# Kernel tuning notes

Measured on AMD Instinct MI355X. Metric: run time of the kernel, lower is better.

Reference implementation:

```python
import jax, jax.numpy as jnp
import numpy as np

S = 2048          # sequence length (single prefill sequence)
HID = 4096        # hidden_size
NH, NKV, HD = 32, 8, 128   # q heads, kv heads, head_dim
THETA = 10000.0
SCALE = HD ** -0.5


def setup_inputs() -> dict:
    key = jax.random.key(0)
    k1, k2, k3 = jax.random.split(key, 3)
    hidden_states = jax.random.normal(k1, (S, HID), jnp.float32)
    positions = jnp.arange(S, dtype=jnp.int32)
    W_qkv = jax.random.normal(k2, (HID, (NH + 2 * NKV) * HD), jnp.float32) * 0.02
    W_o = jax.random.normal(k3, (NH * HD, HID), jnp.float32) * 0.02
    return {"hidden_states": hidden_states, "positions": positions,
            "W_qkv": W_qkv, "W_o": W_o}


def _rope(x, positions):
    # x: [T, H, HD]; neox-style RoPE (rotate halves, is_neox_style=True)
    half = HD // 2
    inv_freq = 1.0 / (THETA ** (jnp.arange(half, dtype=jnp.float32) / half))
    freqs = positions.astype(jnp.float32)[:, None] * inv_freq[None, :]  # [T, half]
    cos = jnp.cos(freqs)[:, None, :]
    sin = jnp.sin(freqs)[:, None, :]
    x1, x2 = x[..., :half], x[..., half:]
    return jnp.concatenate([x1 * cos - x2 * sin, x2 * cos + x1 * sin], axis=-1)


def reference(hidden_states, positions, W_qkv, W_o):
    # fused QKV projection then split (q_size = NH*HD, kv_size = NKV*HD)
    qkv = hidden_states @ W_qkv                      # [S, (NH+2*NKV)*HD]
    q, k, v = jnp.split(qkv, [NH * HD, NH * HD + NKV * HD], axis=1)
    q = _rope(q.reshape(S, NH, HD), positions)       # [S, NH, HD]
    k = _rope(k.reshape(S, NKV, HD), positions)      # [S, NKV, HD]
    v = v.reshape(S, NKV, HD)
    # GQA: broadcast kv heads to query heads
    rep = NH // NKV
    k = jnp.repeat(k, rep, axis=1)                   # [S, NH, HD]
    v = jnp.repeat(v, rep, axis=1)
    scores = jnp.einsum('qhd,khd->hqk', q, k) * SCALE  # [NH, S, S]
    causal = jnp.tril(jnp.ones((S, S), dtype=bool))
    scores = jnp.where(causal[None], scores, jnp.finfo(scores.dtype).min)
    attn = jax.nn.softmax(scores, axis=-1)
    out = jnp.einsum('hqk,khd->qhd', attn, v).reshape(S, NH * HD)
    return out @ W_o                                 # [S, HID]
```

## Files before the change

kernel.cpp:

```cpp
#include <hip/hip_runtime.h>
#include <math.h>
#include <stdint.h>

#define S_LEN 2048
#define HID 4096
#define NH 32
#define NKV 8
#define HD 128
#define QKV_N ((NH + 2*NKV) * HD)
#define NQK (NH + NKV)
static __device__ __constant__ const float SCALE_F = 0.08838834764831845f;

typedef __bf16 bf16x8 __attribute__((ext_vector_type(8)));
typedef __bf16 bf16x4 __attribute__((ext_vector_type(4)));
typedef float  f32x4  __attribute__((ext_vector_type(4)));
typedef uint32_t u32x4 __attribute__((ext_vector_type(4)));

#define GLD_LDS(gptr, lptr) \
  __builtin_amdgcn_global_load_lds( \
      (const __attribute__((address_space(1))) uint32_t*)(gptr), \
      (__attribute__((address_space(3))) uint32_t*)(lptr), 16, 0, 0)

__device__ __forceinline__ void tp64(const float* __restrict__ in, __bf16* __restrict__ out,
                                     int R, int C, int bx, int by, int tid, float* tile) {
  int lr = tid >> 4;
  int lc = (tid & 15) * 4;
  #pragma unroll
  for (int p = 0; p < 4; ++p) {
    int r = p * 16 + lr;
    const float4 v = *(const float4*)&in[(size_t)(by + r) * C + bx + lc];
    float* t = &tile[r * 65 + lc];
    t[0] = v.x; t[1] = v.y; t[2] = v.z; t[3] = v.w;
  }
  __syncthreads();
  int oc = tid >> 5;
  int orr = (tid & 31) * 2;
  #pragma unroll
  for (int p = 0; p < 8; ++p) {
    int c = p * 8 + oc;
    float v0 = tile[orr * 65 + c];
    float v1 = tile[(orr + 1) * 65 + c];
    __bf16 b2[2] = { (__bf16)v0, (__bf16)v1 };
    *(uint32_t*)&out[(size_t)(bx + c) * R + by + orr] = *(uint32_t*)b2;
  }
}

__global__ __launch_bounds__(256) void fused_prep_kernel(const float* __restrict__ hidden,
                                                         __bf16* __restrict__ hid_bf,
                                                         const float* __restrict__ Wqkv,
                                                         __bf16* __restrict__ wqkvT,
                                                         const float* __restrict__ Wo,
                                                         __bf16* __restrict__ woT) {
  __shared__ float tile[64 * 65];
  const int b = blockIdx.x;
  const int tid = threadIdx.x;
  if (b < 2048) {
    const float4* in4 = (const float4*)hidden;
    int i = b * 256 + tid;
    #pragma unroll
    for (int k = 0; k < 4; ++k) {
      float4 v = in4[i + k * 524288];
      bf16x4 o = { (__bf16)v.x, (__bf16)v.y, (__bf16)v.z, (__bf16)v.w };
      *(bf16x4*)(hid_bf + (size_t)(i + k * 524288) * 4) = o;
    }
  } else if (b < 8192) {
    int id = b - 2048;
    int bx = (id % 96) * 64, by = (id / 96) * 64;
    tp64(Wqkv, wqkvT, HID, QKV_N, bx, by, tid, tile);
  } else {
    int id = b - 8192;
    int bx = (id & 63) * 64, by = (id >> 6) * 64;
    tp64(Wo, woT, HID, HID, bx, by, tid, tile);
  }
}

__global__ __launch_bounds__(256) void fused_rope_tpv_kernel(const __bf16* __restrict__ qkv,
                                                             const int* __restrict__ pos,
                                                             __bf16* __restrict__ Qr,
                                                             __bf16* __restrict__ Kr,
                                                             __bf16* __restrict__ Vt) {
  __shared__ __bf16 tile[32][33];
  const int b = blockIdx.x;
  const int tid = threadIdx.x;
  if (b < 20480) {
    int idx = b * 256 + tid;
    int half = idx & 63;
    int t = idx >> 6;
    int hh = t % NQK;
    int s = t / NQK;
    if (s >= S_LEN) return;
    float p = (float)pos[s];
    float inv_freq = exp2f((float)half * -0.2076205059304601f);
    float ang = p * inv_freq;
    float cs = cosf(ang), sn = sinf(ang);
    const __bf16* src; __bf16* dst;
    if (hh < NH) {
      src = qkv + (size_t)s * QKV_N + (size_t)hh * HD;
      dst = Qr + ((size_t)s * NH + hh) * HD;
    } else {
      int kh = hh - NH;
      src = qkv + (size_t)s * QKV_N + (size_t)NH * HD + (size_t)kh * HD;
      dst = Kr + ((size_t)s * NKV + kh) * HD;
    }
    float x1 = (float)src[half], x2 = (float)src[half + 64];
    dst[half]      = (__bf16)(x1 * cs - x2 * sn);
    dst[half + 64] = (__bf16)(x2 * cs + x1 * sn);
  } else {
    int id = b - 20480;
    int sb = (id & 63) * 32;
    int db = ((id >> 6) & 3) * 32;
    int kvh = id >> 8;
    int tx = tid & 31, ty = tid >> 5;
    const __bf16* src = qkv + (size_t)(NH + NKV) * HD + (size_t)kvh * HD;
    for (int i = 0; i < 32; i += 8)
      tile[ty + i][tx] = src[(size_t)(sb + ty + i) * QKV_N + db + tx];
    __syncthreads();
    for (int i = 0; i < 32; i += 8)
      Vt[((size_t)kvh * HD + db + ty + i) * S_LEN + sb + tx] = tile[tx][ty + i];
  }
}

template <typename OutT>
__global__ __launch_bounds__(512, 2) void gemm8p_kernel(const __bf16* __restrict__ A,
                                                        const __bf16* __restrict__ Bt,
                                                        OutT* __restrict__ C0,
                                                        OutT* __restrict__ C1,
                                                        int M, int N, int Kext, int ld) {
  __shared__ __align__(16) __bf16 sA[2][2][256 * 32];
  __shared__ __align__(16) __bf16 sB[2][2][256 * 32];
  const int tid = threadIdx.x;
  const int lane = tid & 63;
  const int wave = tid >> 6;
  const int quad = lane >> 4;
  const int l16 = lane & 15;
  const int wm = (wave >> 2) * 128;
  const int wn = (wave & 3) * 64;

  const int z = blockIdx.z;
  A += (size_t)z * Kext;
  Bt += (size_t)z * Kext;
  OutT* __restrict__ C = z ? C1 : C0;

  const int nx = gridDim.x;
  size_t bm, bn;
  if (gridDim.y == 8 && (nx & 7) == 0) {
    int lin = blockIdx.y * nx + blockIdx.x;
    int j = lin >> 3, xcd = lin & 7;
    bm = (size_t)(j & 7) * 256;
    bn = (size_t)(xcd * (nx >> 3) + (j >> 3)) * 256;
  } else {
    bm = (size_t)blockIdx.y * 256;
    bn = (size_t)blockIdx.x * 256;
  }

  const int NT = Kext >> 6;
  const int rsw = (l16 >> 1) & 3;

  f32x4 acc[8][4] = {};
  bf16x8 aR[2][4], bR[2][4];

  const int row0 = tid >> 2;
  const int chL = (tid & 3) ^ ((tid >> 3) & 3);
  const uint64_t off128 = (uint64_t)128 * ld * 2;
  uint64_t aGA = (uint64_t)(uintptr_t)A + ((bm + row0) * (size_t)ld) * 2 + (size_t)chL * 16;
  uint64_t bGA = (uint64_t)(uintptr_t)Bt + ((bn + row0) * (size_t)ld) * 2 + (size_t)chL * 16;

  typedef __attribute__((address_space(3))) __bf16 lds_bf16;
  const uint32_t sAb = (uint32_t)(uintptr_t)(lds_bf16*)&sA[0][0][0];
  const uint32_t sBb = (uint32_t)(uintptr_t)(lds_bf16*)&sB[0][0][0];
  const uint32_t wlds = (uint32_t)__builtin_amdgcn_readfirstlane(wave * 1024);
  const uint32_t aBase = sAb + (uint32_t)(((wm + l16) * 32 + (quad ^ rsw) * 8) * 2);
  const uint32_t bBase = sBb + (uint32_t)(((wn + l16) * 32 + (quad ^ rsw) * 8) * 2);

#define LDSA(bf, kk) (sAb + (bf) * 32768u + (kk) * 16384u)
#define LDSB(bf, kk) (sBb + (bf) * 32768u + (kk) * 16384u)

#define STAGE_ASM(ga, ldsbase) \
  asm volatile("s_mov_b32 m0, %0\n\t" \
               "global_load_lds_dwordx4 %2, off\n\t" \
               "s_mov_b32 m0, %1\n\t" \
               "global_load_lds_dwordx4 %3, off" \
               :: "s"((ldsbase) + wlds), "s"((ldsbase) + wlds + 8192u), \
                  "v"(ga), "v"((ga) + off128) : "memory")

#define DSRD4(dst, baseaddr) do {                                                 \
    u32x4 t0_, t1_, t2_, t3_;                                                     \
    asm volatile("ds_read_b128 %0, %4\n\t"                                        \
                 "ds_read_b128 %1, %4 offset:1024\n\t"                            \
                 "ds_read_b128 %2, %4 offset:2048\n\t"                            \
                 "ds_read_b128 %3, %4 offset:3072"                                \
                 : "=&v"(t0_), "=&v"(t1_), "=&v"(t2_), "=&v"(t3_)                 \
                 : "v"(baseaddr));                                                \
    dst[0] = __builtin_bit_cast(bf16x8, t0_);                                     \
    dst[1] = __builtin_bit_cast(bf16x8, t1_);                                     \
    dst[2] = __builtin_bit_cast(bf16x8, t2_);                                     \
    dst[3] = __builtin_bit_cast(bf16x8, t3_);                                     \
  } while (0)

#define ISSUE_A(set, bf, kk, ih) DSRD4(aR[set], aBase + (bf) * 32768u + (kk) * 16384u + (ih) * 4096u)
#define ISSUE_B(set, bf, kk)     DSRD4(bR[set], bBase + (bf) * 32768u + (kk) * 16384u)

#define MFMA16(as, bs, ih) do {                                                   \
    __builtin_amdgcn_s_setprio(1);                                                \
    _Pragma("unroll")                                                             \
    for (int i_ = 0; i_ < 4; ++i_)                                                \
      _Pragma("unroll")                                                           \
      for (int j_ = 0; j_ < 4; ++j_)                                              \
        acc[(ih) * 4 + i_][j_] = __builtin_amdgcn_mfma_f32_16x16x32_bf16(         \
            aR[as][i_], bR[bs][j_], acc[(ih) * 4 + i_][j_], 0, 0, 0);             \
    __builtin_amdgcn_s_setprio(0);                                                \
    __builtin_amdgcn_sched_barrier(0);                                            \
  } while (0)

#define BAR() __builtin_amdgcn_s_barrier()
#define LGKM4() do { asm volatile("s_waitcnt lgkmcnt(4)");                        \
                     __builtin_amdgcn_sched_barrier(0); } while (0)
#define LGKM8() do { asm volatile("s_waitcnt lgkmcnt(8)");                        \
                     __builtin_amdgcn_sched_barrier(0); } while (0)
#define VMCNT4() do { asm volatile("s_waitcnt vmcnt(4)");                         \
                      __builtin_amdgcn_sched_barrier(0); } while (0)

  STAGE_ASM(aGA,        LDSA(0, 0));
  STAGE_ASM(bGA,        LDSB(0, 0));
  STAGE_ASM(aGA + 64,   LDSA(0, 1));
  STAGE_ASM(bGA + 64,   LDSB(0, 1));
  STAGE_ASM(aGA + 128,  LDSA(1, 0));
  STAGE_ASM(bGA + 128,  LDSB(1, 0));
  aGA += 192; bGA += 192;
  asm volatile("s_waitcnt vmcnt(8)");
  __builtin_amdgcn_sched_barrier(0);
  BAR();
  ISSUE_A(0, 0, 0, 0); ISSUE_B(0, 0, 0);

  for (int u = 0; u < (NT >> 1); ++u) {
    VMCNT4();
    ISSUE_A(1, 0, 0, 1);
    BAR();
    LGKM4();
    MFMA16(0, 0, 0);
    STAGE_ASM(aGA, LDSA(1, 1)); aGA += 64;
    ISSUE_A(0, 0, 1, 0); ISSUE_B(1, 0, 1);
    BAR();
    LGKM8();
    MFMA16(1, 0, 1);
    STAGE_ASM(bGA, LDSB(1, 1)); bGA += 64;
    VMCNT4();
    ISSUE_A(1, 0, 1, 1);
    BAR();
    LGKM4();
    MFMA16(0, 1, 0);
    STAGE_ASM(aGA, LDSA(0, 0)); aGA += 64;
    ISSUE_A(0, 1, 0, 0); ISSUE_B(0, 1, 0);
    BAR();
    LGKM8();
    MFMA16(1, 1, 1);
    STAGE_ASM(bGA, LDSB(0, 0)); bGA += 64;
    VMCNT4();
    ISSUE_A(1, 1, 0, 1);
    BAR();
    LGKM4();
    MFMA16(0, 0, 0);
    STAGE_ASM(aGA, LDSA(0, 1)); aGA += 64;
    ISSUE_A(0, 1, 1, 0); ISSUE_B(1, 1, 1);
    BAR();
    LGKM8();
    MFMA16(1, 0, 1);
    STAGE_ASM(bGA, LDSB(0, 1)); bGA += 64;
    VMCNT4();
    ISSUE_A(1, 1, 1, 1);
    BAR();
    LGKM4();
    MFMA16(0, 1, 0);
    STAGE_ASM(aGA, LDSA(1, 0)); aGA += 64;
    ISSUE_A(0, 0, 0, 0); ISSUE_B(0, 0, 0);
    BAR();
    LGKM8();
    MFMA16(1, 1, 1);
    STAGE_ASM(bGA, LDSB(1, 0)); bGA += 64;
  }

  asm volatile("s_waitcnt vmcnt(0) lgkmcnt(0)");
  __builtin_amdgcn_sched_barrier(0);

  #pragma unroll
  for (int i = 0; i < 8; ++i)
    #pragma unroll
    for (int j = 0; j < 4; ++j)
      #pragma unroll
      for (int r = 0; r < 4; ++r) {
        size_t row = bm + wm + i * 16 + quad * 4 + r;
        size_t col = bn + wn + j * 16 + l16;
        C[row * (size_t)N + col] = (OutT)acc[i][j][r];
      }

#undef LDSA
#undef LDSB
#undef STAGE_ASM
#undef DSRD4
#undef ISSUE_A
#undef ISSUE_B
#undef MFMA16
#undef BAR
#undef LGKM4
#undef LGKM8
#undef VMCNT4
}

template <typename OutT>
__global__ __launch_bounds__(512, 2) void gemm128_kernel(const __bf16* __restrict__ A,
                                                         const __bf16* __restrict__ Bt,
                                                         OutT* __restrict__ C,
                                                         int M, int N, int K) {
  __shared__ __align__(16) __bf16 sA[3][2][128 * 32];
  __shared__ __align__(16) __bf16 sB[3][2][256 * 32];
  const int tid = threadIdx.x;
  const int lane = tid & 63;
  const int wave = tid >> 6;
  const int quad = lane >> 4;
  const int l16 = lane & 15;
  const int wm = (wave >> 2) * 64;
  const int wn = (wave & 3) * 64;

  const int nx = gridDim.x, ny = gridDim.y;
  const int nwg = nx * ny;
  int lin = blockIdx.y * nx + blockIdx.x;
  size_t bm, bn;
  if ((nwg & 7) == 0) {
    int swz = (lin & 7) * (nwg >> 3) + (lin >> 3);
    bm = (size_t)(swz % ny) * 128;
    bn = (size_t)(swz / ny) * 256;
  } else {
    bm = (size_t)blockIdx.y * 128;
    bn = (size_t)blockIdx.x * 256;
  }

  const int NT = K >> 6;
  const int rsw = (l16 >> 1) & 3;

  f32x4 acc[4][4] = {};
  bf16x8 aR[2][4], bR[2][4];

  const int rowA = tid >> 2;
  const int chLs = (tid & 3) ^ ((tid >> 3) & 3);
  const uint64_t off128B = (uint64_t)128 * K * 2;
  uint64_t aGA = (uint64_t)(uintptr_t)A + ((bm + rowA) * (size_t)K) * 2 + (size_t)chLs * 16;
  uint64_t bGA = (uint64_t)(uintptr_t)Bt + ((bn + rowA) * (size_t)K) * 2 + (size_t)chLs * 16;

  typedef __attribute__((address_space(3))) __bf16 lds_bf16;
  const uint32_t sAb = (uint32_t)(uintptr_t)(lds_bf16*)&sA[0][0][0];
  const uint32_t sBb = (uint32_t)(uintptr_t)(lds_bf16*)&sB[0][0][0];
  const uint32_t wlds = (uint32_t)__builtin_amdgcn_readfirstlane(wave * 1024);
  const uint32_t aBase = sAb + (uint32_t)(((wm + l16) * 32 + (quad ^ rsw) * 8) * 2);
  const uint32_t bBase = sBb + (uint32_t)(((wn + l16) * 32 + (quad ^ rsw) * 8) * 2);

#define STA128(ga, ldsoff) \
  asm volatile("s_mov_b32 m0, %0\n\t" \
               "global_load_lds_dwordx4 %1, off" \
               :: "s"((ldsoff) + wlds), "v"(ga) : "memory")

#define STB128(ga, ldsoff) \
  asm volatile("s_mov_b32 m0, %0\n\t" \
               "global_load_lds_dwordx4 %2, off\n\t" \
               "s_mov_b32 m0, %1\n\t" \
               "global_load_lds_dwordx4 %3, off" \
               :: "s"((ldsoff) + wlds), "s"((ldsoff) + wlds + 8192u), \
                  "v"(ga), "v"((ga) + off128B) : "memory")

#define DSRD4(dst, baseaddr) do {                                                 \
    u32x4 t0_, t1_, t2_, t3_;                                                     \
    asm volatile("ds_read_b128 %0, %4\n\t"                                        \
                 "ds_read_b128 %1, %4 offset:1024\n\t"                            \
                 "ds_read_b128 %2, %4 offset:2048\n\t"                            \
                 "ds_read_b128 %3, %4 offset:3072"                                \
                 : "=&v"(t0_), "=&v"(t1_), "=&v"(t2_), "=&v"(t3_)                 \
                 : "v"(baseaddr));                                                \
    dst[0] = __builtin_bit_cast(bf16x8, t0_);                                     \
    dst[1] = __builtin_bit_cast(bf16x8, t1_);                                     \
    dst[2] = __builtin_bit_cast(bf16x8, t2_);                                     \
    dst[3] = __builtin_bit_cast(bf16x8, t3_);                                     \
  } while (0)

#define IS_A(set, aoff, kh) DSRD4(aR[set], aBase + (aoff) + (kh) * 8192u)
#define IS_B(set, boff, kh) DSRD4(bR[set], bBase + (boff) + (kh) * 16384u)

#define MFMA16Q(ss) do {                                                          \
    __builtin_amdgcn_s_setprio(1);                                                \
    _Pragma("unroll")                                                             \
    for (int i_ = 0; i_ < 4; ++i_)                                                \
      _Pragma("unroll")                                                           \
      for (int j_ = 0; j_ < 4; ++j_)                                              \
        acc[i_][j_] = __builtin_amdgcn_mfma_f32_16x16x32_bf16(                    \
            aR[ss][i_], bR[ss][j_], acc[i_][j_], 0, 0, 0);                        \
    __builtin_amdgcn_s_setprio(0);                                                \
    __builtin_amdgcn_sched_barrier(0);                                            \
  } while (0)

#define BARX() __builtin_amdgcn_s_barrier()
#define LGKM8X() do { asm volatile("s_waitcnt lgkmcnt(8)");                       \
                      __builtin_amdgcn_sched_barrier(0); } while (0)
#define VMCNT6X() do { asm volatile("s_waitcnt vmcnt(6)");                        \
                       __builtin_amdgcn_sched_barrier(0); } while (0)

  uint32_t curA = 0u, nxtA = 16384u, stgA = 32768u;
  uint32_t curB = 0u, nxtB = 32768u, stgB = 65536u;

  STA128(aGA,       sAb + 0u);
  STA128(aGA + 64,  sAb + 8192u);
  STB128(bGA,       sBb + 0u);
  STB128(bGA + 64,  sBb + 16384u);
  STA128(aGA + 128, sAb + 16384u);
  STA128(aGA + 192, sAb + 16384u + 8192u);
  STB128(bGA + 128, sBb + 32768u);
  STB128(bGA + 192, sBb + 32768u + 16384u);
  aGA += 256; bGA += 256;
  VMCNT6X();
  BARX();
  IS_A(0, curA, 0); IS_B(0, curB, 0);

  for (int t = 0; t < NT; ++t) {
    IS_A(1, curA, 1); IS_B(1, curB, 1);
    STA128(aGA, sAb + stgA);
    STB128(bGA, sBb + stgB);
    LGKM8X();
    MFMA16Q(0);
    STA128(aGA + 64, sAb + stgA + 8192u);
    STB128(bGA + 64, sBb + stgB + 16384u);
    aGA += 128; bGA += 128;
    VMCNT6X();
    BARX();
    IS_A(0, nxtA, 0); IS_B(0, nxtB, 0);
    LGKM8X();
    MFMA16Q(1);
    BARX();
    uint32_t ta = curA; curA = nxtA; nxtA = stgA; stgA = ta;
    uint32_t tb = curB; curB = nxtB; nxtB = stgB; stgB = tb;
  }

  asm volatile("s_waitcnt vmcnt(0) lgkmcnt(0)");
  __builtin_amdgcn_sched_barrier(0);

  #pragma unroll
  for (int i = 0; i < 4; ++i)
    #pragma unroll
    for (int j = 0; j < 4; ++j)
      #pragma unroll
      for (int r = 0; r < 4; ++r) {
        size_t row = bm + wm + i * 16 + quad * 4 + r;
        size_t col = bn + wn + j * 16 + l16;
        C[row * (size_t)N + col] = (OutT)acc[i][j][r];
      }

#undef STA128
#undef STB128
#undef DSRD4
#undef IS_A
#undef IS_B
#undef MFMA16Q
#undef BARX
#undef LGKM8X
#undef VMCNT6X
}

__global__ __launch_bounds__(256, 2) void attn_kernel(const __bf16* __restrict__ Qr,
                                                      const __bf16* __restrict__ Kr,
                                                      const __bf16* __restrict__ Vt,
                                                      __bf16* __restrict__ O) {
  __shared__ __align__(16) char smem[73728];
  __bf16* Ps = (__bf16*)(smem + 65536);

  const int bid = blockIdx.x;
  const int h = bid & (NH - 1);
  const int j = bid >> 5;
  const int qb = (j < 8) ? (15 - j) : (j - 8);
  const int kvh = h >> 2;
  const int tid = threadIdx.x;
  const int lane = tid & 63, wave = tid >> 6;
  const int quad = lane >> 4, l16 = lane & 15;
  const int sw = l16 & 7;
  const int q0 = qb * 128;

#define STAGE_KV(kbase, bufv) do {                                                 \
    char* kd_ = smem + (bufv) * 16384;                                             \
    char* vd_ = smem + 32768 + (bufv) * 16384;                                     \
    _Pragma("unroll")                                                              \
    for (int pass_ = 0; pass_ < 4; ++pass_) {                                      \
      int c_ = pass_ * 256 + tid;                                                  \
      int row_ = c_ >> 4, ch_ = c_ & 15;                                           \
      int chs_ = ch_ ^ (row_ & 7);                                                 \
      GLD_LDS(&Kr[(size_t)((kbase) + row_) * (NKV * HD) + (size_t)kvh * HD + chs_ * 8], \
              kd_ + c_ * 16);                                                      \
    }                                                                              \
    _Pragma("unroll")                                                              \
    for (int pass_ = 0; pass_ < 4; ++pass_) {                                      \
      int c_ = pass_ * 256 + tid;                                                  \
      int d_ = c_ >> 3, ch_ = c_ & 7;                                              \
      int chs_ = ch_ ^ (d_ & 7);                                                   \
      GLD_LDS(&Vt[((size_t)kvh * HD + d_) * S_LEN + (kbase) + chs_ * 8],           \
              vd_ + c_ * 16);                                                      \
    }                                                                              \
  } while (0)

#define SOFTMAX_SET(scX, m2X, liX, oaccX, maskCond, pfX) do {                      \
    float s_[16];                                                                  \
    _Pragma("unroll")                                                              \
    for (int jt_ = 0; jt_ < 4; ++jt_)                                              \
      _Pragma("unroll")                                                            \
      for (int r_ = 0; r_ < 4; ++r_) s_[jt_ * 4 + r_] = scX[jt_][r_];              \
    if (maskCond) {                                                                \
      int qloc_ = wave * 16 + l16;                                                 \
      _Pragma("unroll")                                                            \
      for (int jt_ = 0; jt_ < 4; ++jt_)                                            \
        _Pragma("unroll")                                                          \
        for (int r_ = 0; r_ < 4; ++r_)                                             \
          if (jt_ * 16 + quad * 4 + r_ > qloc_) s_[jt_ * 4 + r_] = -INFINITY;      \
    }                                                                              \
    float mx_ = s_[0];                                                             \
    _Pragma("unroll")                                                              \
    for (int i_ = 1; i_ < 16; ++i_) mx_ = fmaxf(mx_, s_[i_]);                      \
    mx_ = fmaxf(mx_, __shfl_xor(mx_, 16, 64));                                     \
    mx_ = fmaxf(mx_, __shfl_xor(mx_, 32, 64));                                     \
    float mxs_ = mx_ * C2;                                                         \
    if (!__all(mxs_ <= m2X + 11.54f)) {                                            \
      float m2n_ = fmaxf(m2X, mxs_);                                               \
      float al_ = exp2f(m2X - m2n_);                                               \
      liX *= al_;                                                                  \
      _Pragma("unroll")                                                            \
      for (int dt_ = 0; dt_ < 8; ++dt_) oaccX[dt_] *= al_;                         \
      m2X = m2n_;                                                                  \
    }                                                                              \
    float sum_ = 0.0f;                                                             \
    __bf16* pw_ = Ps + wave * 1024 + l16 * 64;                                     \
    _Pragma("unroll")                                                              \
    for (int jt_ = 0; jt_ < 4; ++jt_) {                                            \
      float e0_ = exp2f(fmaf(s_[jt_*4+0], C2, -m2X));                              \
      float e1_ = exp2f(fmaf(s_[jt_*4+1], C2, -m2X));                              \
      float e2_ = exp2f(fmaf(s_[jt_*4+2], C2, -m2X));                              \
      float e3_ = exp2f(fmaf(s_[jt_*4+3], C2, -m2X));                              \
      sum_ += (e0_ + e1_) + (e2_ + e3_);                                           \
      bf16x4 pk_ = { (__bf16)e0_, (__bf16)e1_, (__bf16)e2_, (__bf16)e3_ };         \
      int ch_ = jt_ * 2 + (quad >> 1);                                             \
      *(bf16x4*)&pw_[((ch_ ^ sw) * 8) + (quad & 1) * 4] = pk_;                     \
    }                                                                              \
    sum_ += __shfl_xor(sum_, 16, 64);                                              \
    sum_ += __shfl_xor(sum_, 32, 64);                                              \
    liX += sum_;                                                                   \
    pfX[0] = *(const bf16x8*)&pw_[((quad) ^ sw) * 8];                              \
    pfX[1] = *(const bf16x8*)&pw_[((4 + quad) ^ sw) * 8];                          \
  } while (0)

  bf16x8 qf[2][4];
  #pragma unroll
  for (int s2 = 0; s2 < 2; ++s2) {
    const __bf16* qp = Qr + (size_t)(q0 + s2 * 64 + wave * 16 + l16) * (NH * HD)
                          + (size_t)h * HD + quad * 8;
    #pragma unroll
    for (int kk = 0; kk < 4; ++kk) qf[s2][kk] = *(const bf16x8*)(qp + kk * 32);
  }
  f32x4 oacc[2][8] = {};
  float m2[2] = { -INFINITY, -INFINITY }, l_i[2] = { 0.0f, 0.0f };
  const float C2 = SCALE_F * 1.4426950408889634f;
  bf16x8 pf0[2], pf1[2];

  int buf = 0;
  STAGE_KV(0, 0);
  for (int kb = 0; kb <= q0; kb += 64) {
    __syncthreads();
    STAGE_KV(kb + 64, buf ^ 1);

    const __bf16* Ks = (const __bf16*)(smem + buf * 16384);
    const __bf16* Vs = (const __bf16*)(smem + 32768 + buf * 16384);

    f32x4 sc0[4] = {}, sc1[4] = {};
    __builtin_amdgcn_s_setprio(1);
    for (int jt = 0; jt < 4; ++jt)
      for (int kk = 0; kk < 4; ++kk) {
        bf16x8 kf = *(const bf16x8*)&Ks[(jt * 16 + l16) * 128 + ((kk * 4 + quad) ^ sw) * 8];
        sc0[jt] = __builtin_amdgcn_mfma_f32_16x16x32_bf16(kf, qf[0][kk], sc0[jt], 0, 0, 0);
        sc1[jt] = __builtin_amdgcn_mfma_f32_16x16x32_bf16(kf, qf[1][kk], sc1[jt], 0, 0, 0);
      }
    __builtin_amdgcn_s_setprio(0);

    SOFTMAX_SET(sc0, m2[0], l_i[0], oacc[0], (kb == q0), pf0);
    SOFTMAX_SET(sc1, m2[1], l_i[1], oacc[1], false, pf1);

    __builtin_amdgcn_s_setprio(1);
    for (int half = 0; half < 2; ++half)
      for (int dt = 0; dt < 8; ++dt) {
        bf16x8 vf = *(const bf16x8*)&Vs[(dt * 16 + l16) * 64 + ((half * 4 + quad) ^ sw) * 8];
        oacc[0][dt] = __builtin_amdgcn_mfma_f32_16x16x32_bf16(vf, pf0[half], oacc[0][dt], 0, 0, 0);
        oacc[1][dt] = __builtin_amdgcn_mfma_f32_16x16x32_bf16(vf, pf1[half], oacc[1][dt], 0, 0, 0);
      }
    __builtin_amdgcn_s_setprio(0);
    buf ^= 1;
  }
  {
    __syncthreads();
    const __bf16* Ks = (const __bf16*)(smem + buf * 16384);
    const __bf16* Vs = (const __bf16*)(smem + 32768 + buf * 16384);

    f32x4 sc1[4] = {};
    __builtin_amdgcn_s_setprio(1);
    for (int jt = 0; jt < 4; ++jt)
      for (int kk = 0; kk < 4; ++kk) {
        bf16x8 kf = *(const bf16x8*)&Ks[(jt * 16 + l16) * 128 + ((kk * 4 + quad) ^ sw) * 8];
        sc1[jt] = __builtin_amdgcn_mfma_f32_16x16x32_bf16(kf, qf[1][kk], sc1[jt], 0, 0, 0);
      }
    __builtin_amdgcn_s_setprio(0);

    SOFTMAX_SET(sc1, m2[1], l_i[1], oacc[1], true, pf1);

    __builtin_amdgcn_s_setprio(1);
    for (int half = 0; half < 2; ++half)
      for (int dt = 0; dt < 8; ++dt) {
        bf16x8 vf = *(const bf16x8*)&Vs[(dt * 16 + l16) * 64 + ((half * 4 + quad) ^ sw) * 8];
        oacc[1][dt] = __builtin_amdgcn_mfma_f32_16x16x32_bf16(vf, pf1[half], oacc[1][dt], 0, 0, 0);
      }
    __builtin_amdgcn_s_setprio(0);
  }
  __syncthreads();

#undef STAGE_KV
#undef SOFTMAX_SET

  float* scr = (float*)smem + wave * 2112;
  #pragma unroll
  for (int s2 = 0; s2 < 2; ++s2) {
    float inv = 1.0f / l_i[s2];
    #pragma unroll
    for (int dt = 0; dt < 8; ++dt) {
      f32x4 v = oacc[s2][dt] * inv;
      *(f32x4*)&scr[l16 * 132 + dt * 16 + quad * 4] = v;
    }
    #pragma unroll
    for (int it = 0; it < 4; ++it) {
      int c = it * 64 + lane;
      int row = c >> 4, ch = c & 15;
      const float* sp = &scr[row * 132 + ch * 8];
      f32x4 a = *(const f32x4*)sp;
      f32x4 b = *(const f32x4*)(sp + 4);
      bf16x8 o = { (__bf16)a[0], (__bf16)a[1], (__bf16)a[2], (__bf16)a[3],
                   (__bf16)b[0], (__bf16)b[1], (__bf16)b[2], (__bf16)b[3] };
      *(bf16x8*)&O[(size_t)(q0 + s2 * 64 + wave * 16 + row) * (NH * HD)
                   + (size_t)h * HD + ch * 8] = o;
    }
  }
}

extern "C" void kernel_launch(void* const* d_in, const int* in_sizes, int n_in,
                              void* d_out, int out_size, void* d_ws, size_t ws_size,
                              hipStream_t stream) {
  const float* hidden    = (const float*)d_in[0];
  const int*   positions = (const int*)d_in[1];
  const float* Wqkv      = (const float*)d_in[2];
  const float* Wo        = (const float*)d_in[3];
  float* out = (float*)d_out;

  char* p = (char*)d_ws;
  auto alloc = [&](size_t bytes) { char* r = p; p += (bytes + 255) & ~(size_t)255; return r; };
  __bf16* hid_bf = (__bf16*)alloc((size_t)S_LEN * HID * 2);
  __bf16* wqkvT  = (__bf16*)alloc((size_t)QKV_N * HID * 2);
  __bf16* woT    = (__bf16*)alloc((size_t)HID * HID * 2);
  __bf16* qkv    = (__bf16*)alloc((size_t)S_LEN * QKV_N * 2);
  __bf16* Qr     = (__bf16*)alloc((size_t)S_LEN * NH * HD * 2);
  __bf16* Kr     = (__bf16*)alloc((size_t)S_LEN * NKV * HD * 2);
  __bf16* Vt     = (__bf16*)alloc((size_t)S_LEN * NKV * HD * 2);
  __bf16* attn   = hid_bf;

  fused_prep_kernel<<<12288, 256, 0, stream>>>(hidden, hid_bf, Wqkv, wqkvT, Wo, woT);
  gemm8p_kernel<__bf16><<<dim3(QKV_N / 256, S_LEN / 256, 1), 512, 0, stream>>>(
      hid_bf, wqkvT, qkv, qkv, S_LEN, QKV_N, HID, HID);
  fused_rope_tpv_kernel<<<22528, 256, 0, stream>>>(qkv, positions, Qr, Kr, Vt);
  attn_kernel<<<NH * (S_LEN / 128), 256, 0, stream>>>(Qr, Kr, Vt, attn);
  gemm128_kernel<float><<<dim3(HID / 256, S_LEN / 128, 1), 512, 0, stream>>>(
      attn, woT, out, S_LEN, HID, HID);
}
```

Before: 476.7 us.

## Drop register double-buffering of LDS fragments in GEMM kernels, use lgkmcnt(0) waits

```diff
diff --git a/kernel.cpp b/kernel.cpp
--- a/kernel.cpp
+++ b/kernel.cpp
@@ -157,7 +157,7 @@
   const int rsw = (l16 >> 1) & 3;
 
   f32x4 acc[8][4] = {};
-  bf16x8 aR[2][4], bR[2][4];
+  bf16x8 aR[4], bR[4];
 
   const int row0 = tid >> 2;
   const int chL = (tid & 3) ^ ((tid >> 3) & 3);
@@ -197,25 +197,23 @@
     dst[3] = __builtin_bit_cast(bf16x8, t3_);                                     \
   } while (0)
 
-#define ISSUE_A(set, bf, kk, ih) DSRD4(aR[set], aBase + (bf) * 32768u + (kk) * 16384u + (ih) * 4096u)
-#define ISSUE_B(set, bf, kk)     DSRD4(bR[set], bBase + (bf) * 32768u + (kk) * 16384u)
-
-#define MFMA16(as, bs, ih) do {                                                   \
+#define ISSUE_A(bf, kk, ih) DSRD4(aR, aBase + (bf) * 32768u + (kk) * 16384u + (ih) * 4096u)
+#define ISSUE_B(bf, kk)     DSRD4(bR, bBase + (bf) * 32768u + (kk) * 16384u)
+
+#define MFMA16(ih) do {                                                           \
     __builtin_amdgcn_s_setprio(1);                                                \
     _Pragma("unroll")                                                             \
     for (int i_ = 0; i_ < 4; ++i_)                                                \
       _Pragma("unroll")                                                           \
       for (int j_ = 0; j_ < 4; ++j_)                                              \
         acc[(ih) * 4 + i_][j_] = __builtin_amdgcn_mfma_f32_16x16x32_bf16(         \
-            aR[as][i_], bR[bs][j_], acc[(ih) * 4 + i_][j_], 0, 0, 0);             \
+            aR[i_], bR[j_], acc[(ih) * 4 + i_][j_], 0, 0, 0);                     \
     __builtin_amdgcn_s_setprio(0);                                                \
     __builtin_amdgcn_sched_barrier(0);                                            \
   } while (0)
 
 #define BAR() __builtin_amdgcn_s_barrier()
-#define LGKM4() do { asm volatile("s_waitcnt lgkmcnt(4)");                        \
-                     __builtin_amdgcn_sched_barrier(0); } while (0)
-#define LGKM8() do { asm volatile("s_waitcnt lgkmcnt(8)");                        \
+#define LGKM0() do { asm volatile("s_waitcnt lgkmcnt(0)");                        \
                      __builtin_amdgcn_sched_barrier(0); } while (0)
 #define VMCNT4() do { asm volatile("s_waitcnt vmcnt(4)");                         \
                       __builtin_amdgcn_sched_barrier(0); } while (0)
@@ -227,56 +225,36 @@
   STAGE_ASM(aGA + 128,  LDSA(1, 0));
   STAGE_ASM(bGA + 128,  LDSB(1, 0));
   aGA += 192; bGA += 192;
-  asm volatile("s_waitcnt vmcnt(8)");
-  __builtin_amdgcn_sched_barrier(0);
+  VMCNT4();
   BAR();
-  ISSUE_A(0, 0, 0, 0); ISSUE_B(0, 0, 0);
 
   for (int u = 0; u < (NT >> 1); ++u) {
-    VMCNT4();
-    ISSUE_A(1, 0, 0, 1);
-    BAR();
-    LGKM4();
-    MFMA16(0, 0, 0);
+    ISSUE_B(0, 0); ISSUE_A(0, 0, 0);
     STAGE_ASM(aGA, LDSA(1, 1)); aGA += 64;
-    ISSUE_A(0, 0, 1, 0); ISSUE_B(1, 0, 1);
-    BAR();
-    LGKM8();
-    MFMA16(1, 0, 1);
+    BAR(); LGKM0(); MFMA16(0); BAR();
+    ISSUE_A(0, 0, 1);
     STAGE_ASM(bGA, LDSB(1, 1)); bGA += 64;
-    VMCNT4();
-    ISSUE_A(1, 0, 1, 1);
-    BAR();
-    LGKM4();
-    MFMA16(0, 1, 0);
+    BAR(); LGKM0(); MFMA16(1); BAR();
+    ISSUE_B(0, 1); ISSUE_A(0, 1, 0);
     STAGE_ASM(aGA, LDSA(0, 0)); aGA += 64;
-    ISSUE_A(0, 1, 0, 0); ISSUE_B(0, 1, 0);
-    BAR();
-    LGKM8();
-    MFMA16(1, 1, 1);
+    BAR(); LGKM0(); MFMA16(0); BAR();
+    ISSUE_A(0, 1, 1);
     STAGE_ASM(bGA, LDSB(0, 0)); bGA += 64;
     VMCNT4();
-    ISSUE_A(1, 1, 0, 1);
-    BAR();
-    LGKM4();
-    MFMA16(0, 0, 0);
+    BAR(); LGKM0(); MFMA16(1); BAR();
+    ISSUE_B(1, 0); ISSUE_A(1, 0, 0);
     STAGE_ASM(aGA, LDSA(0, 1)); aGA += 64;
-    ISSUE_A(0, 1, 1, 0); ISSUE_B(1, 1, 1);
-    BAR();
-    LGKM8();
-    MFMA16(1, 0, 1);
+    BAR(); LGKM0(); MFMA16(0); BAR();
+    ISSUE_A(1, 0, 1);
     STAGE_ASM(bGA, LDSB(0, 1)); bGA += 64;
+    BAR(); LGKM0(); MFMA16(1); BAR();
+    ISSUE_B(1, 1); ISSUE_A(1, 1, 0);
+    STAGE_ASM(aGA, LDSA(1, 0)); aGA += 64;
+    BAR(); LGKM0(); MFMA16(0); BAR();
+    ISSUE_A(1, 1, 1);
+    STAGE_ASM(bGA, LDSB(1, 0)); bGA += 64;
     VMCNT4();
-    ISSUE_A(1, 1, 1, 1);
-    BAR();
-    LGKM4();
-    MFMA16(0, 1, 0);
-    STAGE_ASM(aGA, LDSA(1, 0)); aGA += 64;
-    ISSUE_A(0, 0, 0, 0); ISSUE_B(0, 0, 0);
-    BAR();
-    LGKM8();
-    MFMA16(1, 1, 1);
-    STAGE_ASM(bGA, LDSB(1, 0)); bGA += 64;
+    BAR(); LGKM0(); MFMA16(1); BAR();
   }
 
   asm volatile("s_waitcnt vmcnt(0) lgkmcnt(0)");
@@ -301,8 +279,7 @@
 #undef ISSUE_B
 #undef MFMA16
 #undef BAR
-#undef LGKM4
-#undef LGKM8
+#undef LGKM0
 #undef VMCNT4
 }
 
@@ -338,7 +315,7 @@
   const int rsw = (l16 >> 1) & 3;
 
   f32x4 acc[4][4] = {};
-  bf16x8 aR[2][4], bR[2][4];
+  bf16x8 aR[4], bR[4];
 
   const int rowA = tid >> 2;
   const int chLs = (tid & 3) ^ ((tid >> 3) & 3);
@@ -380,23 +357,23 @@
     dst[3] = __builtin_bit_cast(bf16x8, t3_);                                     \
   } while (0)
 
-#define IS_A(set, aoff, kh) DSRD4(aR[set], aBase + (aoff) + (kh) * 8192u)
-#define IS_B(set, boff, kh) DSRD4(bR[set], bBase + (boff) + (kh) * 16384u)
-
-#define MFMA16Q(ss) do {                                                          \
+#define IS_A(aoff, kh) DSRD4(aR, aBase + (aoff) + (kh) * 8192u)
+#define IS_B(boff, kh) DSRD4(bR, bBase + (boff) + (kh) * 16384u)
+
+#define MFMA16Q() do {                                                            \
     __builtin_amdgcn_s_setprio(1);                                                \
     _Pragma("unroll")                                                             \
     for (int i_ = 0; i_ < 4; ++i_)                                                \
       _Pragma("unroll")                                                           \
       for (int j_ = 0; j_ < 4; ++j_)                                              \
         acc[i_][j_] = __builtin_amdgcn_mfma_f32_16x16x32_bf16(                    \
-            aR[ss][i_], bR[ss][j_], acc[i_][j_], 0, 0, 0);                        \
+            aR[i_], bR[j_], acc[i_][j_], 0, 0, 0);                                \
     __builtin_amdgcn_s_setprio(0);                                                \
     __builtin_amdgcn_sched_barrier(0);                                            \
   } while (0)
 
 #define BARX() __builtin_amdgcn_s_barrier()
-#define LGKM8X() do { asm volatile("s_waitcnt lgkmcnt(8)");                       \
+#define LGKM0X() do { asm volatile("s_waitcnt lgkmcnt(0)");                       \
                       __builtin_amdgcn_sched_barrier(0); } while (0)
 #define VMCNT6X() do { asm volatile("s_waitcnt vmcnt(6)");                        \
                        __builtin_amdgcn_sched_barrier(0); } while (0)
@@ -415,23 +392,18 @@
   aGA += 256; bGA += 256;
   VMCNT6X();
   BARX();
-  IS_A(0, curA, 0); IS_B(0, curB, 0);
 
   for (int t = 0; t < NT; ++t) {
-    IS_A(1, curA, 1); IS_B(1, curB, 1);
+    IS_A(curA, 0); IS_B(curB, 0);
     STA128(aGA, sAb + stgA);
     STB128(bGA, sBb + stgB);
-    LGKM8X();
-    MFMA16Q(0);
+    BARX(); LGKM0X(); MFMA16Q(); BARX();
+    IS_A(curA, 1); IS_B(curB, 1);
     STA128(aGA + 64, sAb + stgA + 8192u);
     STB128(bGA + 64, sBb + stgB + 16384u);
     aGA += 128; bGA += 128;
     VMCNT6X();
-    BARX();
-    IS_A(0, nxtA, 0); IS_B(0, nxtB, 0);
-    LGKM8X();
-    MFMA16Q(1);
-    BARX();
+    BARX(); LGKM0X(); MFMA16Q(); BARX();
     uint32_t ta = curA; curA = nxtA; nxtA = stgA; stgA = ta;
     uint32_t tb = curB; curB = nxtB; nxtB = stgB; stgB = tb;
   }
@@ -457,7 +429,7 @@
 #undef IS_B
 #undef MFMA16Q
 #undef BARX
-#undef LGKM8X
+#undef LGKM0X
 #undef VMCNT6X
 }
 
```

Measured after the change: 483.1 us. About the same (+1.3%).

## Move Wo transpose into attention tail and simplify gemm128 register pipeline

Applied to the files above, without the earlier changes.

```diff
diff --git a/kernel.cpp b/kernel.cpp
--- a/kernel.cpp
+++ b/kernel.cpp
@@ -48,9 +48,7 @@
 __global__ __launch_bounds__(256) void fused_prep_kernel(const float* __restrict__ hidden,
                                                          __bf16* __restrict__ hid_bf,
                                                          const float* __restrict__ Wqkv,
-                                                         __bf16* __restrict__ wqkvT,
-                                                         const float* __restrict__ Wo,
-                                                         __bf16* __restrict__ woT) {
+                                                         __bf16* __restrict__ wqkvT) {
   __shared__ float tile[64 * 65];
   const int b = blockIdx.x;
   const int tid = threadIdx.x;
@@ -63,14 +61,10 @@
       bf16x4 o = { (__bf16)v.x, (__bf16)v.y, (__bf16)v.z, (__bf16)v.w };
       *(bf16x4*)(hid_bf + (size_t)(i + k * 524288) * 4) = o;
     }
-  } else if (b < 8192) {
+  } else {
     int id = b - 2048;
     int bx = (id % 96) * 64, by = (id / 96) * 64;
     tp64(Wqkv, wqkvT, HID, QKV_N, bx, by, tid, tile);
-  } else {
-    int id = b - 8192;
-    int bx = (id & 63) * 64, by = (id >> 6) * 64;
-    tp64(Wo, woT, HID, HID, bx, by, tid, tile);
   }
 }
 
@@ -338,7 +332,7 @@
   const int rsw = (l16 >> 1) & 3;
 
   f32x4 acc[4][4] = {};
-  bf16x8 aR[2][4], bR[2][4];
+  bf16x8 aR[4], bR[4];
 
   const int rowA = tid >> 2;
   const int chLs = (tid & 3) ^ ((tid >> 3) & 3);
@@ -380,23 +374,23 @@
     dst[3] = __builtin_bit_cast(bf16x8, t3_);                                     \
   } while (0)
 
-#define IS_A(set, aoff, kh) DSRD4(aR[set], aBase + (aoff) + (kh) * 8192u)
-#define IS_B(set, boff, kh) DSRD4(bR[set], bBase + (boff) + (kh) * 16384u)
-
-#define MFMA16Q(ss) do {                                                          \
+#define IS_A(aoff, kh) DSRD4(aR, aBase + (aoff) + (kh) * 8192u)
+#define IS_B(boff, kh) DSRD4(bR, bBase + (boff) + (kh) * 16384u)
+
+#define MFMA16Q() do {                                                            \
     __builtin_amdgcn_s_setprio(1);                                                \
     _Pragma("unroll")                                                             \
     for (int i_ = 0; i_ < 4; ++i_)                                                \
       _Pragma("unroll")                                                           \
       for (int j_ = 0; j_ < 4; ++j_)                                              \
         acc[i_][j_] = __builtin_amdgcn_mfma_f32_16x16x32_bf16(                    \
-            aR[ss][i_], bR[ss][j_], acc[i_][j_], 0, 0, 0);                        \
+            aR[i_], bR[j_], acc[i_][j_], 0, 0, 0);                                \
     __builtin_amdgcn_s_setprio(0);                                                \
     __builtin_amdgcn_sched_barrier(0);                                            \
   } while (0)
 
 #define BARX() __builtin_amdgcn_s_barrier()
-#define LGKM8X() do { asm volatile("s_waitcnt lgkmcnt(8)");                       \
+#define LGKM0X() do { asm volatile("s_waitcnt lgkmcnt(0)");                       \
                       __builtin_amdgcn_sched_barrier(0); } while (0)
 #define VMCNT6X() do { asm volatile("s_waitcnt vmcnt(6)");                        \
                        __builtin_amdgcn_sched_barrier(0); } while (0)
@@ -415,23 +409,18 @@
   aGA += 256; bGA += 256;
   VMCNT6X();
   BARX();
-  IS_A(0, curA, 0); IS_B(0, curB, 0);
 
   for (int t = 0; t < NT; ++t) {
-    IS_A(1, curA, 1); IS_B(1, curB, 1);
+    IS_A(curA, 0); IS_B(curB, 0);
     STA128(aGA, sAb + stgA);
     STB128(bGA, sBb + stgB);
-    LGKM8X();
-    MFMA16Q(0);
+    BARX(); LGKM0X(); MFMA16Q(); BARX();
+    IS_A(curA, 1); IS_B(curB, 1);
     STA128(aGA + 64, sAb + stgA + 8192u);
     STB128(bGA + 64, sBb + stgB + 16384u);
     aGA += 128; bGA += 128;
     VMCNT6X();
-    BARX();
-    IS_A(0, nxtA, 0); IS_B(0, nxtB, 0);
-    LGKM8X();
-    MFMA16Q(1);
-    BARX();
+    BARX(); LGKM0X(); MFMA16Q(); BARX();
     uint32_t ta = curA; curA = nxtA; nxtA = stgA; stgA = ta;
     uint32_t tb = curB; curB = nxtB; nxtB = stgB; stgB = tb;
   }
@@ -457,23 +446,32 @@
 #undef IS_B
 #undef MFMA16Q
 #undef BARX
-#undef LGKM8X
+#undef LGKM0X
 #undef VMCNT6X
 }
 
 __global__ __launch_bounds__(256, 2) void attn_kernel(const __bf16* __restrict__ Qr,
                                                       const __bf16* __restrict__ Kr,
                                                       const __bf16* __restrict__ Vt,
-                                                      __bf16* __restrict__ O) {
+                                                      __bf16* __restrict__ O,
+                                                      const float* __restrict__ Wo,
+                                                      __bf16* __restrict__ woT) {
   __shared__ __align__(16) char smem[73728];
   __bf16* Ps = (__bf16*)(smem + 65536);
 
   const int bid = blockIdx.x;
+  const int tid = threadIdx.x;
+  if (bid >= 512) {
+    int id = bid - 512;
+    int bx = (id & 63) * 64, by = (id >> 6) * 64;
+    tp64(Wo, woT, HID, HID, bx, by, tid, (float*)smem);
+    return;
+  }
+
   const int h = bid & (NH - 1);
   const int j = bid >> 5;
   const int qb = (j < 8) ? (15 - j) : (j - 8);
   const int kvh = h >> 2;
-  const int tid = threadIdx.x;
   const int lane = tid & 63, wave = tid >> 6;
   const int quad = lane >> 4, l16 = lane & 15;
   const int sw = l16 & 7;
@@ -666,11 +664,11 @@
   __bf16* Vt     = (__bf16*)alloc((size_t)S_LEN * NKV * HD * 2);
   __bf16* attn   = hid_bf;
 
-  fused_prep_kernel<<<12288, 256, 0, stream>>>(hidden, hid_bf, Wqkv, wqkvT, Wo, woT);
+  fused_prep_kernel<<<8192, 256, 0, stream>>>(hidden, hid_bf, Wqkv, wqkvT);
   gemm8p_kernel<__bf16><<<dim3(QKV_N / 256, S_LEN / 256, 1), 512, 0, stream>>>(
       hid_bf, wqkvT, qkv, qkv, S_LEN, QKV_N, HID, HID);
   fused_rope_tpv_kernel<<<22528, 256, 0, stream>>>(qkv, positions, Qr, Kr, Vt);
-  attn_kernel<<<NH * (S_LEN / 128), 256, 0, stream>>>(Qr, Kr, Vt, attn);
+  attn_kernel<<<512 + 4096, 256, 0, stream>>>(Qr, Kr, Vt, attn, Wo, woT);
   gemm128_kernel<float><<<dim3(HID / 256, S_LEN / 128, 1), 512, 0, stream>>>(
       attn, woT, out, S_LEN, HID, HID);
 }
```

New measurement: 451.3 us. 1.06x faster.
